# Kernel optimization log

Hardware: AMD Instinct MI355X
Metric: run time of the kernel (lower is better)

## Reference

```python
import jax, jax.numpy as jnp
import numpy as np

N = 50000
E = 800000
FEAT = 512
HID = 256
CLS = 40
EPS = 1e-5


def setup_inputs() -> dict:
    key = jax.random.key(0)
    ks = jax.random.split(key, 8)
    x = jax.random.normal(ks[0], (N, FEAT), dtype=jnp.float32)
    edge_index = jax.random.randint(ks[1], (2, E), 0, N, dtype=jnp.int64)
    s = 0.05
    return {
        "x": x,
        "edge_index": edge_index,
        "W1": jax.random.normal(ks[2], (FEAT, HID), dtype=jnp.float32) * s,
        "b1": jnp.zeros((HID,), jnp.float32),
        "W2": jax.random.normal(ks[3], (HID, HID), dtype=jnp.float32) * s,
        "b2": jnp.zeros((HID,), jnp.float32),
        "W3": jax.random.normal(ks[4], (HID, CLS), dtype=jnp.float32) * s,
        "b3": jnp.zeros((CLS,), jnp.float32),
        "gamma": jnp.ones((HID,), jnp.float32),
        "beta": jnp.zeros((HID,), jnp.float32),
        "run_mean": jnp.zeros((HID,), jnp.float32),
        "run_var": jnp.ones((HID,), jnp.float32),
    }


def _edge_norm(edge_index):
    # add self-loops, then symmetric normalization D^-1/2 (A+I) D^-1/2
    loop = jnp.arange(N, dtype=edge_index.dtype)
    src = jnp.concatenate([edge_index[0], loop])
    dst = jnp.concatenate([edge_index[1], loop])
    deg = jax.ops.segment_sum(jnp.ones_like(dst, jnp.float32), dst, num_segments=N)
    inv_sqrt = jnp.where(deg > 0, jax.lax.rsqrt(jnp.maximum(deg, 1.0)), 0.0)
    norm = inv_sqrt[src] * inv_sqrt[dst]  # [E+N]
    return src, dst, norm


def _gcn_conv(x, W, b, src, dst, norm):
    h = x @ W                               # [N, out]
    msg = h[src] * norm[:, None]            # gather + scale, [E+N, out]
    out = jax.ops.segment_sum(msg, dst, num_segments=N)
    return out + b


def _bn_relu(x, gamma, beta, mean, var):
    return jax.nn.relu((x - mean) * jax.lax.rsqrt(var + EPS) * gamma + beta)


def reference(x, edge_index, W1, b1, W2, b2, W3, b3, gamma, beta, run_mean, run_var):
    src, dst, norm = _edge_norm(edge_index)
    h = _gcn_conv(x, W1, b1, src, dst, norm)
    h = _bn_relu(h, gamma, beta, run_mean, run_var)
    h = _gcn_conv(h, W2, b2, src, dst, norm)
    h = _bn_relu(h, gamma, beta, run_mean, run_var)
    h = _gcn_conv(h, W3, b3, src, dst, norm)
    return h
```

## Files before the change

### kernel.cpp

```cpp
#include <hip/hip_runtime.h>
#include <cstdint>
#include <cstddef>

#define FEAT 512
#define HID 256
#define CLS 40
#define EPS 1e-5f

typedef __attribute__((ext_vector_type(8))) short short8;
typedef __attribute__((ext_vector_type(4))) float f32x4v;


__device__ __forceinline__ unsigned short f2bf(float f) {
    union { float f; unsigned u; } v; v.f = f;
    unsigned r = v.u + 0x7FFF + ((v.u >> 16) & 1);
    return (unsigned short)(r >> 16);
}
__device__ __forceinline__ float bf2f(unsigned short h) {
    union { unsigned u; float f; } v; v.u = ((unsigned)h) << 16;
    return v.f;
}

typedef const __attribute__((address_space(1))) unsigned int* gas_ptr;
typedef __attribute__((address_space(3))) unsigned int* las_ptr;
__device__ __forceinline__ void lds_load16(const void* g, void* l) {
    __builtin_amdgcn_global_load_lds((gas_ptr)g, (las_ptr)l, 16, 0, 0);
}

__device__ __forceinline__ float4 f4add(float4 a, float4 b) {
    return make_float4(a.x + b.x, a.y + b.y, a.z + b.z, a.w + b.w);
}

__device__ __forceinline__ void accum_bf4(float4& a, ushort4 v) {
    a.x += bf2f(v.x); a.y += bf2f(v.y); a.z += bf2f(v.z); a.w += bf2f(v.w);
}


__global__ void zero_kernel(int* counts, int* fillpos, int n) {
    int i = blockIdx.x * 256 + threadIdx.x;
    if (i < n) { counts[i] = 0; fillpos[i] = 0; }
}

__global__ void hist_kernel(const int* __restrict__ dst, int* __restrict__ counts, int E) {
    int e = blockIdx.x * 256 + threadIdx.x;
    if (e < E) atomicAdd(&counts[dst[e]], 1);
}

__global__ void scan_block_kernel(const int* __restrict__ counts, int* __restrict__ row_ptr,
                                  int* __restrict__ blocksums, int n) {
    __shared__ int s[256];
    int tid = threadIdx.x;
    int i = blockIdx.x * 256 + tid;
    int v = (i < n) ? counts[i] : 0;
    s[tid] = v; __syncthreads();
    for (int off = 1; off < 256; off <<= 1) {
        int t = (tid >= off) ? s[tid - off] : 0;
        __syncthreads();
        s[tid] += t;
        __syncthreads();
    }
    if (i < n) row_ptr[i] = s[tid] - v;
    if (tid == 255) blocksums[blockIdx.x] = s[255];
}

__global__ void scan_sums_kernel(const int* __restrict__ blocksums, int* __restrict__ blockoffs, int nb) {
    __shared__ int s[256];
    int tid = threadIdx.x;
    int v = (tid < nb) ? blocksums[tid] : 0;
    s[tid] = v; __syncthreads();
    for (int off = 1; off < 256; off <<= 1) {
        int t = (tid >= off) ? s[tid - off] : 0;
        __syncthreads();
        s[tid] += t;
        __syncthreads();
    }
    blockoffs[tid] = s[tid] - v;
}

__global__ void finalize_rowptr_kernel(int* __restrict__ row_ptr, const int* __restrict__ blockoffs,
                                       const int* __restrict__ counts, float* __restrict__ inv_sqrt,
                                       int n, int E) {
    int i = blockIdx.x * 256 + threadIdx.x;
    if (i < n) {
        row_ptr[i] += blockoffs[i >> 8];
        inv_sqrt[i] = rsqrtf((float)(counts[i] + 1));
    }
    if (i == 0) row_ptr[n] = E;
}

__global__ void fill_kernel(const int* __restrict__ src, const int* __restrict__ dst,
                            const int* __restrict__ row_ptr, int* __restrict__ fillpos,
                            int* __restrict__ src_sorted, int E) {
    int e = blockIdx.x * 256 + threadIdx.x;
    if (e < E) {
        int d = dst[e];
        int pos = row_ptr[d] + atomicAdd(&fillpos[d], 1);
        src_sorted[pos] = src[e];
    }
}


__global__ void cvt_w_kernel(const float* __restrict__ W, unsigned short* __restrict__ hi,
                             unsigned short* __restrict__ lo, int K, int Ncol) {
    int idx = blockIdx.x * 256 + threadIdx.x;
    if (idx >= K * Ncol) return;
    int k = idx / Ncol, n = idx % Ncol;
    float f = W[idx];
    unsigned short h = f2bf(f);
    hi[(size_t)n * K + k] = h;
    lo[(size_t)n * K + k] = f2bf(f - bf2f(h));
}


__global__ __launch_bounds__(256) void cvt_x_kernel(const float* __restrict__ x,
                                                    unsigned short* __restrict__ out, int total8) {
    int i = blockIdx.x * 256 + threadIdx.x;
    if (i >= total8) return;
    const float4* xp = (const float4*)x;
    float4 a = xp[2 * i], b = xp[2 * i + 1];
    float f[8] = {a.x, a.y, a.z, a.w, b.x, b.y, b.z, b.w};
    short8 h;
#pragma unroll
    for (int j = 0; j < 8; ++j) h[j] = (short)f2bf(f[j]);
    ((short8*)out)[i] = h;
}


template<bool A_SPLIT, int BK>
__global__ __launch_bounds__(256) void gemm_mfma_kernel(
        const unsigned short* __restrict__ gAhi, const unsigned short* __restrict__ gAlo,
        const unsigned short* __restrict__ Wthi, const unsigned short* __restrict__ Wtlo,
        const float* __restrict__ inv_sqrt, unsigned short* __restrict__ C,
        int M, int K, int Ncol) {
    constexpr int BLK = 16 * BK;
    __shared__ unsigned short AhiL[128 * BK];
    __shared__ unsigned short AloL[A_SPLIT ? 128 * BK : 4];
    __shared__ unsigned short BhiL[128 * BK], BloL[128 * BK];
    const int tid  = threadIdx.x;
    const int lane = tid & 63;
    const int w    = tid >> 6;
    const int wr   = w >> 1, wc = w & 1;
    const int lm   = lane & 15;
    const int lk8  = (lane >> 4) * 8;
    const int bm   = blockIdx.x * 128;
    const int bn   = blockIdx.y * 128;

    f32x4v acc[4][4] = {};

    int nc0 = bn + 16 * (2 * w) + lm;
    int nc1 = bn + 16 * (2 * w + 1) + lm;
    const unsigned short* gB_h0 = Wthi + (size_t)nc0 * K + lk8;
    const unsigned short* gB_h1 = Wthi + (size_t)nc1 * K + lk8;
    const unsigned short* gB_l0 = Wtlo + (size_t)nc0 * K + lk8;
    const unsigned short* gB_l1 = Wtlo + (size_t)nc1 * K + lk8;

    int ar0 = bm + 16 * (2 * w) + lm;     if (ar0 >= M) ar0 = M - 1;
    int ar1 = bm + 16 * (2 * w + 1) + lm; if (ar1 >= M) ar1 = M - 1;
    const unsigned short* gA_h0 = gAhi + (size_t)ar0 * K + lk8;
    const unsigned short* gA_h1 = gAhi + (size_t)ar1 * K + lk8;
    const unsigned short* gA_l0 = A_SPLIT ? gAlo + (size_t)ar0 * K + lk8 : nullptr;
    const unsigned short* gA_l1 = A_SPLIT ? gAlo + (size_t)ar1 * K + lk8 : nullptr;

    for (int k0 = 0; k0 < K; k0 += BK) {
#pragma unroll
        for (int kk = 0; kk < BK / 32; ++kk) {
            const int kg = k0 + 32 * kk;
            const int lo = kk * 512;
            lds_load16(gA_h0 + kg, &AhiL[(2 * w) * BLK + lo]);
            lds_load16(gA_h1 + kg, &AhiL[(2 * w + 1) * BLK + lo]);
            if (A_SPLIT) {
                lds_load16(gA_l0 + kg, &AloL[(2 * w) * BLK + lo]);
                lds_load16(gA_l1 + kg, &AloL[(2 * w + 1) * BLK + lo]);
            }
            lds_load16(gB_h0 + kg, &BhiL[(2 * w) * BLK + lo]);
            lds_load16(gB_h1 + kg, &BhiL[(2 * w + 1) * BLK + lo]);
            lds_load16(gB_l0 + kg, &BloL[(2 * w) * BLK + lo]);
            lds_load16(gB_l1 + kg, &BloL[(2 * w + 1) * BLK + lo]);
        }
        __syncthreads();

#pragma unroll
        for (int half = 0; half < BK / 32; ++half) {
            const int ho = half * 512;
            short8 ah[4], av[4], bh[4], bv[4];
#pragma unroll
            for (int i = 0; i < 4; ++i) {
                int ao = (wr * 4 + i) * BLK + ho + lane * 8;
                int bo = (wc * 4 + i) * BLK + ho + lane * 8;
                ah[i] = *(const short8*)&AhiL[ao];
                if (A_SPLIT) av[i] = *(const short8*)&AloL[ao];
                bh[i] = *(const short8*)&BhiL[bo];
                bv[i] = *(const short8*)&BloL[bo];
            }
#pragma unroll
            for (int i = 0; i < 4; ++i)
#pragma unroll
                for (int j = 0; j < 4; ++j) {
                    acc[i][j] = __builtin_amdgcn_mfma_f32_16x16x32_bf16(ah[i], bh[j], acc[i][j], 0, 0, 0);
                    if (A_SPLIT)
                        acc[i][j] = __builtin_amdgcn_mfma_f32_16x16x32_bf16(av[i], bh[j], acc[i][j], 0, 0, 0);
                    acc[i][j] = __builtin_amdgcn_mfma_f32_16x16x32_bf16(ah[i], bv[j], acc[i][j], 0, 0, 0);
                }
        }
        __syncthreads();
    }

    const int orow_base = bm + wr * 64;
    const int ocol_base = bn + wc * 64 + lm;
    const int rq = (lane >> 4) * 4;
#pragma unroll
    for (int i = 0; i < 4; ++i) {
#pragma unroll
        for (int r = 0; r < 4; ++r) {
            int row = orow_base + i * 16 + rq + r;
            if (row >= M) continue;
            float s = inv_sqrt[row];
            size_t rb = (size_t)row * Ncol;
#pragma unroll
            for (int j = 0; j < 4; ++j)
                C[rb + ocol_base + j * 16] = f2bf(acc[i][j][r] * s);
        }
    }
}


__global__ __launch_bounds__(256) void gemm_scaled_hl_kernel(
        const unsigned short* __restrict__ Ahi, const unsigned short* __restrict__ Alo,
        const float* __restrict__ W,
        const float* __restrict__ inv_sqrt, float* __restrict__ C,
        int M, int K, int Ncol) {
    __shared__ float As[16][64];
    __shared__ float Ws[16][64];
    int tid = threadIdx.x;
    int tm = tid >> 4;
    int tn = tid & 15;
    int bm = blockIdx.x * 64;
    int bn = blockIdx.y * 64;

    float acc[4][4] = {};

    int lr = tid >> 2;
    int lc = (tid & 3) << 2;
    int wr = tid >> 4;
    int wc = (tid & 15) << 2;
    int arow = bm + lr;
    bool aok = arow < M;
    bool wok = (bn + wc) < Ncol;
    const unsigned short* AhiRow = Ahi + (size_t)arow * K + lc;
    const unsigned short* AloRow = Alo + (size_t)arow * K + lc;

    for (int k0 = 0; k0 < K; k0 += 16) {
        float4 av = make_float4(0.f, 0.f, 0.f, 0.f);
        if (aok) {
            ushort4 hv = *(const ushort4*)(AhiRow + k0);
            ushort4 lv = *(const ushort4*)(AloRow + k0);
            av.x = bf2f(hv.x) + bf2f(lv.x);
            av.y = bf2f(hv.y) + bf2f(lv.y);
            av.z = bf2f(hv.z) + bf2f(lv.z);
            av.w = bf2f(hv.w) + bf2f(lv.w);
        }
        As[lc + 0][lr] = av.x; As[lc + 1][lr] = av.y;
        As[lc + 2][lr] = av.z; As[lc + 3][lr] = av.w;

        float4 wv = make_float4(0.f, 0.f, 0.f, 0.f);
        if (wok) wv = *(const float4*)(W + (size_t)(k0 + wr) * Ncol + bn + wc);
        *(float4*)&Ws[wr][wc] = wv;
        __syncthreads();

#pragma unroll
        for (int k = 0; k < 16; ++k) {
            const float4 a4 = *(const float4*)&As[k][tm << 2];
            const float4 b4 = *(const float4*)&Ws[k][tn << 2];
            float a[4] = {a4.x, a4.y, a4.z, a4.w};
            float b[4] = {b4.x, b4.y, b4.z, b4.w};
#pragma unroll
            for (int i = 0; i < 4; ++i)
#pragma unroll
                for (int j = 0; j < 4; ++j)
                    acc[i][j] = fmaf(a[i], b[j], acc[i][j]);
        }
        __syncthreads();
    }

#pragma unroll
    for (int i = 0; i < 4; ++i) {
        int row = bm + (tm << 2) + i;
        if (row >= M) continue;
        float s = inv_sqrt[row];
        int col = bn + (tn << 2);
        if (col < Ncol) {
            float4 o = make_float4(acc[i][0] * s, acc[i][1] * s, acc[i][2] * s, acc[i][3] * s);
            *(float4*)&C[(size_t)row * Ncol + col] = o;
        }
    }
}


__global__ __launch_bounds__(256) void agg_bn_hl_kernel(
        const unsigned short* __restrict__ g, const int* __restrict__ row_ptr,
        const int* __restrict__ srcs, const float* __restrict__ inv_sqrt,
        const float* __restrict__ bias, const float* __restrict__ gamma,
        const float* __restrict__ beta, const float* __restrict__ mean,
        const float* __restrict__ var,
        unsigned short* __restrict__ out_hi, unsigned short* __restrict__ out_lo, int n) {
    int node = (blockIdx.x << 2) + (threadIdx.x >> 6);
    int lane = threadIdx.x & 63;
    if (node >= n) return;
    const ushort4* gp = (const ushort4*)g;
    float4 acc0 = make_float4(0.f, 0.f, 0.f, 0.f);
    float4 acc1 = make_float4(0.f, 0.f, 0.f, 0.f);
    accum_bf4(acc0, gp[(size_t)node * 64 + lane]);
    int beg = row_ptr[node];
    int cnt = row_ptr[node + 1] - beg;

    for (int base = 0; base < cnt; base += 64) {
        int m = cnt - base; if (m > 64) m = 64;
        int idx = (lane < m) ? srcs[beg + base + lane] : 0;
        int j = 0;
        for (; j + 8 <= m; j += 8) {
            int s0 = __shfl(idx, j + 0), s1 = __shfl(idx, j + 1);
            int s2 = __shfl(idx, j + 2), s3 = __shfl(idx, j + 3);
            int s4 = __shfl(idx, j + 4), s5 = __shfl(idx, j + 5);
            int s6 = __shfl(idx, j + 6), s7 = __shfl(idx, j + 7);
            ushort4 v0 = gp[(size_t)s0 * 64 + lane];
            ushort4 v1 = gp[(size_t)s1 * 64 + lane];
            ushort4 v2 = gp[(size_t)s2 * 64 + lane];
            ushort4 v3 = gp[(size_t)s3 * 64 + lane];
            ushort4 v4 = gp[(size_t)s4 * 64 + lane];
            ushort4 v5 = gp[(size_t)s5 * 64 + lane];
            ushort4 v6 = gp[(size_t)s6 * 64 + lane];
            ushort4 v7 = gp[(size_t)s7 * 64 + lane];
            accum_bf4(acc0, v0); accum_bf4(acc0, v1);
            accum_bf4(acc0, v2); accum_bf4(acc0, v3);
            accum_bf4(acc1, v4); accum_bf4(acc1, v5);
            accum_bf4(acc1, v6); accum_bf4(acc1, v7);
        }
        for (; j < m; ++j) {
            int s = __shfl(idx, j);
            accum_bf4(acc0, gp[(size_t)s * 64 + lane]);
        }
    }
    float4 acc = f4add(acc0, acc1);

    float inv = inv_sqrt[node];
    float4 b4  = ((const float4*)bias)[lane];
    float4 ga4 = ((const float4*)gamma)[lane];
    float4 be4 = ((const float4*)beta)[lane];
    float4 m4  = ((const float4*)mean)[lane];
    float4 v4  = ((const float4*)var)[lane];
    float4 o;
    o.x = fmaxf((acc.x * inv + b4.x - m4.x) * (ga4.x * rsqrtf(v4.x + EPS)) + be4.x, 0.f);
    o.y = fmaxf((acc.y * inv + b4.y - m4.y) * (ga4.y * rsqrtf(v4.y + EPS)) + be4.y, 0.f);
    o.z = fmaxf((acc.z * inv + b4.z - m4.z) * (ga4.z * rsqrtf(v4.z + EPS)) + be4.z, 0.f);
    o.w = fmaxf((acc.w * inv + b4.w - m4.w) * (ga4.w * rsqrtf(v4.w + EPS)) + be4.w, 0.f);
    ushort4 oh, ol;
    oh.x = f2bf(o.x); ol.x = f2bf(o.x - bf2f(oh.x));
    oh.y = f2bf(o.y); ol.y = f2bf(o.y - bf2f(oh.y));
    oh.z = f2bf(o.z); ol.z = f2bf(o.z - bf2f(oh.z));
    oh.w = f2bf(o.w); ol.w = f2bf(o.w - bf2f(oh.w));
    ((ushort4*)out_hi)[(size_t)node * 64 + lane] = oh;
    ((ushort4*)out_lo)[(size_t)node * 64 + lane] = ol;
}


__global__ __launch_bounds__(256) void agg_final_kernel(
        const float* __restrict__ g, const int* __restrict__ row_ptr,
        const int* __restrict__ srcs, const float* __restrict__ inv_sqrt,
        const float* __restrict__ bias, float* __restrict__ out, int n) {
    int node = (blockIdx.x << 2) + (threadIdx.x >> 6);
    int lane = threadIdx.x & 63;
    if (node >= n) return;
    int flane = (lane < CLS) ? lane : 0;
    float acc0 = g[(size_t)node * CLS + flane];
    float acc1 = 0.f;
    int beg = row_ptr[node];
    int cnt = row_ptr[node + 1] - beg;

    for (int base = 0; base < cnt; base += 64) {
        int m = cnt - base; if (m > 64) m = 64;
        int idx = (lane < m) ? srcs[beg + base + lane] : 0;
        int j = 0;
        for (; j + 8 <= m; j += 8) {
            int s0 = __shfl(idx, j + 0), s1 = __shfl(idx, j + 1);
            int s2 = __shfl(idx, j + 2), s3 = __shfl(idx, j + 3);
            int s4 = __shfl(idx, j + 4), s5 = __shfl(idx, j + 5);
            int s6 = __shfl(idx, j + 6), s7 = __shfl(idx, j + 7);
            float v0 = g[(size_t)s0 * CLS + flane];
            float v1 = g[(size_t)s1 * CLS + flane];
            float v2 = g[(size_t)s2 * CLS + flane];
            float v3 = g[(size_t)s3 * CLS + flane];
            float v4 = g[(size_t)s4 * CLS + flane];
            float v5 = g[(size_t)s5 * CLS + flane];
            float v6 = g[(size_t)s6 * CLS + flane];
            float v7 = g[(size_t)s7 * CLS + flane];
            acc0 += (v0 + v1) + (v2 + v3);
            acc1 += (v4 + v5) + (v6 + v7);
        }
        for (; j < m; ++j) {
            int s = __shfl(idx, j);
            acc0 += g[(size_t)s * CLS + flane];
        }
    }
    if (lane < CLS)
        out[(size_t)node * CLS + lane] = (acc0 + acc1) * inv_sqrt[node] + bias[lane];
}


extern "C" void kernel_launch(void* const* d_in, const int* in_sizes, int n_in,
                              void* d_out, int out_size, void* d_ws, size_t ws_size,
                              hipStream_t stream) {
    const float* x     = (const float*)d_in[0];
    const int*   edges = (const int*)d_in[1];
    const float* W1    = (const float*)d_in[2];
    const float* b1    = (const float*)d_in[3];
    const float* W2    = (const float*)d_in[4];
    const float* b2    = (const float*)d_in[5];
    const float* W3    = (const float*)d_in[6];
    const float* b3    = (const float*)d_in[7];
    const float* gamma = (const float*)d_in[8];
    const float* beta  = (const float*)d_in[9];
    const float* mean  = (const float*)d_in[10];
    const float* var   = (const float*)d_in[11];

    const int N = in_sizes[0] / FEAT;
    const int E = in_sizes[1] / 2;
    const int* src = edges;
    const int* dst = edges + E;

    char* ws = (char*)d_ws;
    auto alloc = [&](size_t bytes) -> char* {
        char* p = ws;
        ws += (bytes + 255) & ~(size_t)255;
        return p;
    };
    int*   counts     = (int*)  alloc((size_t)N * 4);
    int*   fillpos    = (int*)  alloc((size_t)N * 4);
    int*   row_ptr    = (int*)  alloc((size_t)(N + 1) * 4);
    int*   blocksums  = (int*)  alloc(256 * 4);
    int*   blockoffs  = (int*)  alloc(256 * 4);
    float* inv_sqrt   = (float*)alloc((size_t)N * 4);
    int*   src_sorted = (int*)  alloc((size_t)E * 4);
    unsigned short* w1hi = (unsigned short*)alloc((size_t)FEAT * HID * 2);
    unsigned short* w1lo = (unsigned short*)alloc((size_t)FEAT * HID * 2);
    unsigned short* w2hi = (unsigned short*)alloc((size_t)HID * HID * 2);
    unsigned short* w2lo = (unsigned short*)alloc((size_t)HID * HID * 2);
    unsigned short* g    = (unsigned short*)alloc((size_t)N * HID * 2);
    unsigned short* h_hi = (unsigned short*)alloc((size_t)N * HID * 2);
    unsigned short* h_lo = (unsigned short*)alloc((size_t)N * HID * 2);
    unsigned short* xbf  = h_hi;

    int nb = (N + 255) / 256;
    int eb = (E + 255) / 256;

    zero_kernel<<<nb, 256, 0, stream>>>(counts, fillpos, N);
    hist_kernel<<<eb, 256, 0, stream>>>(dst, counts, E);
    scan_block_kernel<<<nb, 256, 0, stream>>>(counts, row_ptr, blocksums, N);
    scan_sums_kernel<<<1, 256, 0, stream>>>(blocksums, blockoffs, nb);
    finalize_rowptr_kernel<<<nb, 256, 0, stream>>>(row_ptr, blockoffs, counts, inv_sqrt, N, E);
    fill_kernel<<<eb, 256, 0, stream>>>(src, dst, row_ptr, fillpos, src_sorted, E);

    cvt_w_kernel<<<(FEAT * HID + 255) / 256, 256, 0, stream>>>(W1, w1hi, w1lo, FEAT, HID);
    cvt_w_kernel<<<(HID * HID + 255) / 256, 256, 0, stream>>>(W2, w2hi, w2lo, HID, HID);
    int total8 = N * FEAT / 8;
    cvt_x_kernel<<<(total8 + 255) / 256, 256, 0, stream>>>(x, xbf, total8);

    dim3 mfma_grid((N + 127) / 128, HID / 128);
    dim3 gemm3_grid((N + 63) / 64, 1);
    dim3 agg_grid((N + 3) / 4);

    gemm_mfma_kernel<false, 64><<<mfma_grid, 256, 0, stream>>>(
        xbf, nullptr, w1hi, w1lo, inv_sqrt, g, N, FEAT, HID);
    agg_bn_hl_kernel<<<agg_grid, 256, 0, stream>>>(g, row_ptr, src_sorted, inv_sqrt,
                                                   b1, gamma, beta, mean, var, h_hi, h_lo, N);
    gemm_mfma_kernel<true, 32><<<mfma_grid, 256, 0, stream>>>(
        h_hi, h_lo, w2hi, w2lo, inv_sqrt, g, N, HID, HID);
    agg_bn_hl_kernel<<<agg_grid, 256, 0, stream>>>(g, row_ptr, src_sorted, inv_sqrt,
                                                   b2, gamma, beta, mean, var, h_hi, h_lo, N);
    float* g3 = (float*)g;
    gemm_scaled_hl_kernel<<<gemm3_grid, 256, 0, stream>>>(h_hi, h_lo, W3, inv_sqrt, g3, N, HID, CLS);
    agg_final_kernel<<<agg_grid, 256, 0, stream>>>(g3, row_ptr, src_sorted, inv_sqrt,
                                                   b3, (float*)d_out, N);
}
```

Baseline: 558.2 us.

## Merge prep kernels, fold block-sum scan into finalize, drop layer-2 A lo split

The zero, weight-conversion and x-conversion kernels are merged into one flat-indexed prep kernel, and the single-block scan of block sums moves into every block of finalize_rowptr, which removes launches. The layer-1 aggregation now writes only the bf16 high part, and the layer-2 GEMM runs with A_SPLIT=false and BK=64. That removes the lo-part writes and reads and the extra MFMA passes on A. The cost is lower precision on the hidden activations fed into layer 2.

```diff
diff --git a/kernel.cpp b/kernel.cpp
--- a/kernel.cpp
+++ b/kernel.cpp
@@ -36,10 +36,48 @@
 }
 
 
-__global__ void zero_kernel(int* counts, int* fillpos, int n) {
+__global__ __launch_bounds__(256) void prep_cvt_kernel(
+        const float* __restrict__ x, const float* __restrict__ W1, const float* __restrict__ W2,
+        int* __restrict__ counts, int* __restrict__ fillpos,
+        unsigned short* __restrict__ w1hi, unsigned short* __restrict__ w1lo,
+        unsigned short* __restrict__ w2hi, unsigned short* __restrict__ w2lo,
+        unsigned short* __restrict__ xbf, int N) {
     int i = blockIdx.x * 256 + threadIdx.x;
-    if (i < n) { counts[i] = 0; fillpos[i] = 0; }
-}
+    const int n0 = N;
+    const int n1 = FEAT * HID;
+    const int n2 = HID * HID;
+    const int n3 = N * FEAT / 8;
+    if (i < n0) { counts[i] = 0; fillpos[i] = 0; return; }
+    i -= n0;
+    if (i < n1) {
+        int k = i / HID, n = i % HID;
+        float f = W1[i];
+        unsigned short h = f2bf(f);
+        w1hi[(size_t)n * FEAT + k] = h;
+        w1lo[(size_t)n * FEAT + k] = f2bf(f - bf2f(h));
+        return;
+    }
+    i -= n1;
+    if (i < n2) {
+        int k = i / HID, n = i % HID;
+        float f = W2[i];
+        unsigned short h = f2bf(f);
+        w2hi[(size_t)n * HID + k] = h;
+        w2lo[(size_t)n * HID + k] = f2bf(f - bf2f(h));
+        return;
+    }
+    i -= n2;
+    if (i < n3) {
+        const float4* xp = (const float4*)x;
+        float4 a = xp[2 * i], b = xp[2 * i + 1];
+        float f[8] = {a.x, a.y, a.z, a.w, b.x, b.y, b.z, b.w};
+        short8 h;
+#pragma unroll
+        for (int j = 0; j < 8; ++j) h[j] = (short)f2bf(f[j]);
+        ((short8*)xbf)[i] = h;
+    }
+}
+
 
 __global__ void hist_kernel(const int* __restrict__ dst, int* __restrict__ counts, int E) {
     int e = blockIdx.x * 256 + threadIdx.x;
@@ -63,8 +101,11 @@
     if (tid == 255) blocksums[blockIdx.x] = s[255];
 }
 
-__global__ void scan_sums_kernel(const int* __restrict__ blocksums, int* __restrict__ blockoffs, int nb) {
+__global__ void finalize_rowptr_kernel(int* __restrict__ row_ptr, const int* __restrict__ blocksums,
+                                       const int* __restrict__ counts, float* __restrict__ inv_sqrt,
+                                       int n, int E, int nb) {
     __shared__ int s[256];
+    __shared__ int excl[256];
     int tid = threadIdx.x;
     int v = (tid < nb) ? blocksums[tid] : 0;
     s[tid] = v; __syncthreads();
@@ -74,15 +115,11 @@
         s[tid] += t;
         __syncthreads();
     }
-    blockoffs[tid] = s[tid] - v;
-}
-
-__global__ void finalize_rowptr_kernel(int* __restrict__ row_ptr, const int* __restrict__ blockoffs,
-                                       const int* __restrict__ counts, float* __restrict__ inv_sqrt,
-                                       int n, int E) {
-    int i = blockIdx.x * 256 + threadIdx.x;
+    excl[tid] = s[tid] - v;
+    __syncthreads();
+    int i = blockIdx.x * 256 + tid;
     if (i < n) {
-        row_ptr[i] += blockoffs[i >> 8];
+        row_ptr[i] += excl[i >> 8];
         inv_sqrt[i] = rsqrtf((float)(counts[i] + 1));
     }
     if (i == 0) row_ptr[n] = E;
@@ -97,32 +134,6 @@
         int pos = row_ptr[d] + atomicAdd(&fillpos[d], 1);
         src_sorted[pos] = src[e];
     }
-}
-
-
-__global__ void cvt_w_kernel(const float* __restrict__ W, unsigned short* __restrict__ hi,
-                             unsigned short* __restrict__ lo, int K, int Ncol) {
-    int idx = blockIdx.x * 256 + threadIdx.x;
-    if (idx >= K * Ncol) return;
-    int k = idx / Ncol, n = idx % Ncol;
-    float f = W[idx];
-    unsigned short h = f2bf(f);
-    hi[(size_t)n * K + k] = h;
-    lo[(size_t)n * K + k] = f2bf(f - bf2f(h));
-}
-
-
-__global__ __launch_bounds__(256) void cvt_x_kernel(const float* __restrict__ x,
-                                                    unsigned short* __restrict__ out, int total8) {
-    int i = blockIdx.x * 256 + threadIdx.x;
-    if (i >= total8) return;
-    const float4* xp = (const float4*)x;
-    float4 a = xp[2 * i], b = xp[2 * i + 1];
-    float f[8] = {a.x, a.y, a.z, a.w, b.x, b.y, b.z, b.w};
-    short8 h;
-#pragma unroll
-    for (int j = 0; j < 8; ++j) h[j] = (short)f2bf(f[j]);
-    ((short8*)out)[i] = h;
 }
 
 
@@ -296,6 +307,7 @@
 }
 
 
+template<bool WRITE_LO>
 __global__ __launch_bounds__(256) void agg_bn_hl_kernel(
         const unsigned short* __restrict__ g, const int* __restrict__ row_ptr,
         const int* __restrict__ srcs, const float* __restrict__ inv_sqrt,
@@ -353,13 +365,17 @@
     o.y = fmaxf((acc.y * inv + b4.y - m4.y) * (ga4.y * rsqrtf(v4.y + EPS)) + be4.y, 0.f);
     o.z = fmaxf((acc.z * inv + b4.z - m4.z) * (ga4.z * rsqrtf(v4.z + EPS)) + be4.z, 0.f);
     o.w = fmaxf((acc.w * inv + b4.w - m4.w) * (ga4.w * rsqrtf(v4.w + EPS)) + be4.w, 0.f);
-    ushort4 oh, ol;
-    oh.x = f2bf(o.x); ol.x = f2bf(o.x - bf2f(oh.x));
-    oh.y = f2bf(o.y); ol.y = f2bf(o.y - bf2f(oh.y));
-    oh.z = f2bf(o.z); ol.z = f2bf(o.z - bf2f(oh.z));
-    oh.w = f2bf(o.w); ol.w = f2bf(o.w - bf2f(oh.w));
+    ushort4 oh;
+    oh.x = f2bf(o.x); oh.y = f2bf(o.y); oh.z = f2bf(o.z); oh.w = f2bf(o.w);
     ((ushort4*)out_hi)[(size_t)node * 64 + lane] = oh;
-    ((ushort4*)out_lo)[(size_t)node * 64 + lane] = ol;
+    if (WRITE_LO) {
+        ushort4 ol;
+        ol.x = f2bf(o.x - bf2f(oh.x));
+        ol.y = f2bf(o.y - bf2f(oh.y));
+        ol.z = f2bf(o.z - bf2f(oh.z));
+        ol.w = f2bf(o.w - bf2f(oh.w));
+        ((ushort4*)out_lo)[(size_t)node * 64 + lane] = ol;
+    }
 }
 
 
@@ -437,7 +453,6 @@
     int*   fillpos    = (int*)  alloc((size_t)N * 4);
     int*   row_ptr    = (int*)  alloc((size_t)(N + 1) * 4);
     int*   blocksums  = (int*)  alloc(256 * 4);
-    int*   blockoffs  = (int*)  alloc(256 * 4);
     float* inv_sqrt   = (float*)alloc((size_t)N * 4);
     int*   src_sorted = (int*)  alloc((size_t)E * 4);
     unsigned short* w1hi = (unsigned short*)alloc((size_t)FEAT * HID * 2);
@@ -452,17 +467,13 @@
     int nb = (N + 255) / 256;
     int eb = (E + 255) / 256;
 
-    zero_kernel<<<nb, 256, 0, stream>>>(counts, fillpos, N);
+    int prep_items = N + FEAT * HID + HID * HID + N * FEAT / 8;
+    prep_cvt_kernel<<<(prep_items + 255) / 256, 256, 0, stream>>>(
+        x, W1, W2, counts, fillpos, w1hi, w1lo, w2hi, w2lo, xbf, N);
     hist_kernel<<<eb, 256, 0, stream>>>(dst, counts, E);
     scan_block_kernel<<<nb, 256, 0, stream>>>(counts, row_ptr, blocksums, N);
-    scan_sums_kernel<<<1, 256, 0, stream>>>(blocksums, blockoffs, nb);
-    finalize_rowptr_kernel<<<nb, 256, 0, stream>>>(row_ptr, blockoffs, counts, inv_sqrt, N, E);
+    finalize_rowptr_kernel<<<nb, 256, 0, stream>>>(row_ptr, blocksums, counts, inv_sqrt, N, E, nb);
     fill_kernel<<<eb, 256, 0, stream>>>(src, dst, row_ptr, fillpos, src_sorted, E);
-
-    cvt_w_kernel<<<(FEAT * HID + 255) / 256, 256, 0, stream>>>(W1, w1hi, w1lo, FEAT, HID);
-    cvt_w_kernel<<<(HID * HID + 255) / 256, 256, 0, stream>>>(W2, w2hi, w2lo, HID, HID);
-    int total8 = N * FEAT / 8;
-    cvt_x_kernel<<<(total8 + 255) / 256, 256, 0, stream>>>(x, xbf, total8);
 
     dim3 mfma_grid((N + 127) / 128, HID / 128);
     dim3 gemm3_grid((N + 63) / 64, 1);
@@ -470,12 +481,12 @@
 
     gemm_mfma_kernel<false, 64><<<mfma_grid, 256, 0, stream>>>(
         xbf, nullptr, w1hi, w1lo, inv_sqrt, g, N, FEAT, HID);
-    agg_bn_hl_kernel<<<agg_grid, 256, 0, stream>>>(g, row_ptr, src_sorted, inv_sqrt,
-                                                   b1, gamma, beta, mean, var, h_hi, h_lo, N);
-    gemm_mfma_kernel<true, 32><<<mfma_grid, 256, 0, stream>>>(
-        h_hi, h_lo, w2hi, w2lo, inv_sqrt, g, N, HID, HID);
-    agg_bn_hl_kernel<<<agg_grid, 256, 0, stream>>>(g, row_ptr, src_sorted, inv_sqrt,
-                                                   b2, gamma, beta, mean, var, h_hi, h_lo, N);
+    agg_bn_hl_kernel<false><<<agg_grid, 256, 0, stream>>>(g, row_ptr, src_sorted, inv_sqrt,
+                                                          b1, gamma, beta, mean, var, h_hi, nullptr, N);
+    gemm_mfma_kernel<false, 64><<<mfma_grid, 256, 0, stream>>>(
+        h_hi, nullptr, w2hi, w2lo, inv_sqrt, g, N, HID, HID);
+    agg_bn_hl_kernel<true><<<agg_grid, 256, 0, stream>>>(g, row_ptr, src_sorted, inv_sqrt,
+                                                         b2, gamma, beta, mean, var, h_hi, h_lo, N);
     float* g3 = (float*)g;
     gemm_scaled_hl_kernel<<<gemm3_grid, 256, 0, stream>>>(h_hi, h_lo, W3, inv_sqrt, g3, N, HID, CLS);
     agg_final_kernel<<<agg_grid, 256, 0, stream>>>(g3, row_ptr, src_sorted, inv_sqrt,
```

Measured after the change: 540.1 us. -3.2%, faster.
